# Kernel tuning notes

Hardware: AMD Instinct MI355X
Metric: run time of the kernel (lower is better)

## Reference

```python
import jax, jax.numpy as jnp
import numpy as np
import math

H = 128          # num heads
D = 5120         # hidden
Q_LORA = 1536
KV_LORA = 512    # nope_size / latent dim
ROPE = 64        # qk_rope_head_dim
NOPE = 128       # qk_nope_head_dim
VDIM = 128       # v_head_dim
Q_HEAD = NOPE + ROPE  # 192
EPS = 1e-6
_MSCALE = 0.1 * 1.0 * math.log(40.0) + 1.0
SCALE = (Q_HEAD ** -0.5) * _MSCALE * _MSCALE


def rmsnorm(x, w):
    var = jnp.mean(x.astype(jnp.float32) ** 2, axis=-1, keepdims=True)
    return (x * jax.lax.rsqrt(var + EPS)).astype(x.dtype) * w


def rotate_half(x):
    h = x.shape[-1] // 2
    return jnp.concatenate([-x[..., h:], x[..., :h]], axis=-1)


def apply_rope(x, cos, sin):
    return x * cos + rotate_half(x) * sin


def setup_inputs() -> dict:
    key = jax.random.key(0)
    ks = jax.random.split(key, 12)
    S = 1024
    s = 0.02
    return {
        'hidden_states': jax.random.normal(ks[0], (1, S, D), jnp.float32),
        'cos': jax.random.uniform(ks[1], (S, ROPE), jnp.float32, -1.0, 1.0),
        'sin': jax.random.uniform(ks[2], (S, ROPE), jnp.float32, -1.0, 1.0),
        'q_a_w': jax.random.normal(ks[3], (D, Q_LORA), jnp.float32) * s,
        'q_a_ln_w': jnp.ones((Q_LORA,), jnp.float32),
        'q_b_w': jax.random.normal(ks[4], (Q_LORA, H * Q_HEAD), jnp.float32) * s,
        'kv_a_w': jax.random.normal(ks[5], (D, KV_LORA + ROPE), jnp.float32) * s,
        'kv_a_ln_w': jnp.ones((KV_LORA,), jnp.float32),
        'kc_w': jax.random.normal(ks[6], (H, NOPE, KV_LORA), jnp.float32) * s,
        'vc_w': jax.random.normal(ks[7], (H, KV_LORA, VDIM), jnp.float32) * s,
        'o_w': jax.random.normal(ks[8], (H * VDIM, D), jnp.float32) * s,
    }


def reference(hidden_states, cos, sin, q_a_w, q_a_ln_w, q_b_w, kv_a_w,
              kv_a_ln_w, kc_w, vc_w, o_w):
    h = hidden_states[0]                     # [S, D]
    S = h.shape[0]

    # --- q path: low-rank q with RMSNorm, then absorbed nope proj via per-head bmm
    q = rmsnorm(h @ q_a_w, q_a_ln_w) @ q_b_w  # [S, H*192]
    q = q.reshape(S, H, Q_HEAD)
    q_nope, q_pe = q[..., :NOPE], q[..., NOPE:]         # [S,H,128], [S,H,64]
    q_nope_abs = jnp.einsum('shd,hdl->shl', q_nope, kc_w)  # [S,H,512] (kc bmm)

    # --- kv path: shared latent (MQA, 1 kv head)
    kv = h @ kv_a_w                          # [S, 512+64]
    k_pe = kv[:, KV_LORA:]                   # [S, 64]
    latent = rmsnorm(kv[:, :KV_LORA], kv_a_ln_w)  # [S, 512] = value states

    # --- partial RoPE on the 64-dim pe slice only
    q_pe = apply_rope(q_pe, cos[:, None, :], sin[:, None, :])
    k_pe = apply_rope(k_pe, cos, sin)

    q_full = jnp.concatenate([q_nope_abs, q_pe], axis=-1)  # [S,H,576]
    k_full = jnp.concatenate([latent, k_pe], axis=-1)      # [S,576]

    # --- causal MLA attention in latent space (values = 512-dim latent)
    scores = jnp.einsum('qhd,kd->hqk', q_full, k_full) * SCALE  # [H,S,S]
    causal = jnp.tril(jnp.ones((S, S), bool))
    scores = jnp.where(causal[None], scores, jnp.finfo(scores.dtype).min)
    probs = jax.nn.softmax(scores, axis=-1)
    attn = jnp.einsum('hqk,kl->qhl', probs, latent)         # [S,H,512]

    # --- vc bmm back to v_head_dim, then output proj
    out = jnp.einsum('shl,hlv->shv', attn, vc_w)            # [S,H,128]
    out = out.reshape(S, H * VDIM) @ o_w                    # [S, D]
    return out[None]                                        # [1,S,D]
```

## Files before the change

### kernel.cpp

```cpp
#include <hip/hip_runtime.h>
#include <hip/hip_bf16.h>
#include <math.h>

#define S_LEN  1024
#define DMODEL 5120
#define QLORA  1536
#define KVLORA 512
#define ROPE_D 64
#define NOPE_D 128
#define VDIM_D 128
#define QHEAD  192
#define NHEAD  128

typedef __hip_bfloat16 bf16;

using bf16x8 = __attribute__((ext_vector_type(8))) __bf16;
using f32x4  = __attribute__((ext_vector_type(4))) float;

__device__ __forceinline__ float toF(float x) { return x; }
__device__ __forceinline__ float toF(bf16 x)  { return __bfloat162float(x); }

__device__ __forceinline__ bf16x8 ld8(const bf16* p) {
  return *reinterpret_cast<const bf16x8*>(p);
}

__global__ __launch_bounds__(256) void cvt_bf16(const float* __restrict__ in,
                                                bf16* __restrict__ out) {
  const int i = (blockIdx.x * 256 + threadIdx.x) * 4;
  const float4 v = *reinterpret_cast<const float4*>(in + i);
  out[i + 0] = __float2bfloat16(v.x);
  out[i + 1] = __float2bfloat16(v.y);
  out[i + 2] = __float2bfloat16(v.z);
  out[i + 3] = __float2bfloat16(v.w);
}

__global__ __launch_bounds__(256) void transpose_w(const float* __restrict__ in,
                                                   bf16* __restrict__ out,
                                                   int R, int C) {
  __shared__ float tile[32][33];
  const int h = blockIdx.z;
  const int c0 = blockIdx.x * 32, r0 = blockIdx.y * 32;
  const int rr = threadIdx.x >> 3, cc = (threadIdx.x & 7) * 4;
  const float* ip = in + ((size_t)h * R + r0 + rr) * C + c0 + cc;
#pragma unroll
  for (int i = 0; i < 4; ++i) tile[rr][cc + i] = ip[i];
  __syncthreads();
  bf16* op = out + ((size_t)h * C + c0 + rr) * R + r0 + cc;
#pragma unroll
  for (int i = 0; i < 4; ++i) op[i] = __float2bfloat16(tile[cc + i][rr]);
}

template<int MODE>
__global__ __launch_bounds__(256) void gemm_mfma(const bf16* __restrict__ A,
                                                 const bf16* __restrict__ BT,
                                                 void* __restrict__ Cout,
                                                 int M, int N, int K) {
  __shared__ bf16 As[128][72];
  __shared__ bf16 Bs[128][72];
  const int n0 = blockIdx.x * 128, m0 = blockIdx.y * 128;
  const int tid = threadIdx.x;
  const int w = tid >> 6, l = tid & 63, lr = l & 15, lg = l >> 4;
  const int wr = w >> 1, wc = w & 1;

  f32x4 acc[4][4];
#pragma unroll
  for (int x = 0; x < 4; ++x)
#pragma unroll
    for (int y = 0; y < 4; ++y) acc[x][y] = (f32x4){0.f, 0.f, 0.f, 0.f};

  for (int kk = 0; kk < K; kk += 64) {
#pragma unroll
    for (int i = 0; i < 4; ++i) {
      const int e = tid + 256 * i;
      const int r = e >> 3, k8 = (e & 7) * 8;
      *reinterpret_cast<bf16x8*>(&As[r][k8]) =
          ld8(A + (size_t)(m0 + r) * K + kk + k8);
      const int bn = (n0 + r < N) ? n0 + r : N - 1;
      *reinterpret_cast<bf16x8*>(&Bs[r][k8]) =
          ld8(BT + (size_t)bn * K + kk + k8);
    }
    __syncthreads();
#pragma unroll
    for (int kh = 0; kh < 2; ++kh) {
      bf16x8 af[4], bg[4];
#pragma unroll
      for (int x = 0; x < 4; ++x) af[x] = ld8(&As[wr * 64 + x * 16 + lr][kh * 32 + lg * 8]);
#pragma unroll
      for (int y = 0; y < 4; ++y) bg[y] = ld8(&Bs[wc * 64 + y * 16 + lr][kh * 32 + lg * 8]);
#pragma unroll
      for (int x = 0; x < 4; ++x)
#pragma unroll
        for (int y = 0; y < 4; ++y)
          acc[x][y] = __builtin_amdgcn_mfma_f32_16x16x32_bf16(af[x], bg[y], acc[x][y], 0, 0, 0);
    }
    __syncthreads();
  }

#pragma unroll
  for (int x = 0; x < 4; ++x) {
    const int mb = m0 + wr * 64 + x * 16 + lg * 4;
#pragma unroll
    for (int y = 0; y < 4; ++y) {
      const int n = n0 + wc * 64 + y * 16 + lr;
      if (n < N) {
#pragma unroll
        for (int i = 0; i < 4; ++i) {
          const int m = mb + i;
          if (MODE == 0) {
            ((float*)Cout)[(size_t)m * N + n] = acc[x][y][i];
          } else if (MODE == 1) {
            ((bf16*)Cout)[(size_t)m * N + n] = __float2bfloat16(acc[x][y][i]);
          } else {
            const int h = n / QHEAD, j = n - h * QHEAD;
            ((bf16*)Cout)[((size_t)h * S_LEN + m) * QHEAD + j] = __float2bfloat16(acc[x][y][i]);
          }
        }
      }
    }
  }
}

__global__ __launch_bounds__(256) void rmsnorm_kernel(const bf16* __restrict__ in,
                                                      const float* __restrict__ w,
                                                      bf16* __restrict__ out, int N) {
  const int row = blockIdx.x, tid = threadIdx.x;
  __shared__ float red[256];
  float ss = 0.f;
  for (int c = tid; c < N; c += 256) { float x = toF(in[(size_t)row * N + c]); ss += x * x; }
  red[tid] = ss; __syncthreads();
  for (int s = 128; s > 0; s >>= 1) { if (tid < s) red[tid] += red[tid + s]; __syncthreads(); }
  const float rs = rsqrtf(red[0] / (float)N + 1e-6f);
  for (int c = tid; c < N; c += 256) {
    float x = toF(in[(size_t)row * N + c]);
    out[(size_t)row * N + c] = __float2bfloat16(x * rs * w[c]);
  }
}

__global__ __launch_bounds__(256) void kfull_kernel(const float* __restrict__ kv,
                                                    const float* __restrict__ w,
                                                    const float* __restrict__ cosb,
                                                    const float* __restrict__ sinb,
                                                    bf16* __restrict__ kfull) {
  const int s = blockIdx.x, tid = threadIdx.x;
  __shared__ float red[256];
  const float* row = kv + (size_t)s * 576;
  const float x0 = row[tid], x1 = row[256 + tid];
  red[tid] = x0 * x0 + x1 * x1; __syncthreads();
  for (int t = 128; t > 0; t >>= 1) { if (tid < t) red[tid] += red[tid + t]; __syncthreads(); }
  const float rs = rsqrtf(red[0] / 512.f + 1e-6f);
  bf16* krow = kfull + (size_t)s * 576;
  krow[tid]       = __float2bfloat16(x0 * rs * w[tid]);
  krow[256 + tid] = __float2bfloat16(x1 * rs * w[256 + tid]);
  if (tid < 32) {
    const int j = tid;
    const float a = row[512 + j], b = row[544 + j];
    const float* cs = cosb + (size_t)s * 64;
    const float* sn = sinb + (size_t)s * 64;
    krow[512 + j] = __float2bfloat16(a * cs[j] - b * sn[j]);
    krow[544 + j] = __float2bfloat16(b * cs[32 + j] + a * sn[32 + j]);
  }
}

__global__ __launch_bounds__(256) void rope_q_kernel(bf16* __restrict__ qperm,
                                                     const float* __restrict__ cosb,
                                                     const float* __restrict__ sinb) {
  const int idx = blockIdx.x * 256 + threadIdx.x;
  const int h = idx >> 15;
  const int rem = idx & 32767;
  const int s = rem >> 5;
  const int j = rem & 31;
  bf16* base = qperm + ((size_t)h * S_LEN + s) * QHEAD + NOPE_D;
  const float a = toF(base[j]), b = toF(base[32 + j]);
  const float* cs = cosb + (size_t)s * 64;
  const float* sn = sinb + (size_t)s * 64;
  base[j]      = __float2bfloat16(a * cs[j] - b * sn[j]);
  base[32 + j] = __float2bfloat16(b * cs[32 + j] + a * sn[32 + j]);
}

__global__ __launch_bounds__(256) void latT_kernel(const bf16* __restrict__ kfull,
                                                   bf16* __restrict__ latT) {
  const int gid = blockIdx.x * 256 + threadIdx.x;
  const int v = gid >> 10, s = gid & 1023;
  latT[gid] = kfull[(size_t)s * 576 + v];
}

#define QB 32
__global__ __launch_bounds__(256, 3) void attn_mfma(const bf16* __restrict__ qperm,
                                                    const bf16* __restrict__ kfull,
                                                    const bf16* __restrict__ kcT,
                                                    const bf16* __restrict__ vcT,
                                                    const bf16* __restrict__ latT,
                                                    bf16* __restrict__ attnv,
                                                    float scale) {
  const int bi = blockIdx.x;
  const int y  = bi >> 3;
  const int h  = (bi & 7) * 16 + (y >> 5);
  const int qb = y & 31;
  const int r0 = qb * QB;
  const int tid = threadIdx.x;
  const int w = tid >> 6, l = tid & 63, lr = l & 15, lg = l >> 4;

  __shared__ bf16  Qf[QB][584];
  __shared__ float St[QB][68];
  __shared__ bf16  Pt[QB][72];
  __shared__ float mrow[QB], lrow[QB], arow[QB];

  for (int e = tid; e < QB * 64; e += 256) {
    const int i = e >> 6, j = e & 63;
    Qf[i][512 + j] = qperm[((size_t)h * S_LEN + r0 + i) * QHEAD + NOPE_D + j];
  }
  {
    bf16x8 qn[2][4];
#pragma unroll
    for (int x = 0; x < 2; ++x) {
      const bf16* qp = qperm + ((size_t)h * S_LEN + r0 + x * 16 + lr) * QHEAD;
#pragma unroll
      for (int t = 0; t < 4; ++t) qn[x][t] = ld8(qp + t * 32 + lg * 8);
    }
#pragma unroll
    for (int ff = 0; ff < 2; ++ff) {
      bf16x8 kb[4][4];
#pragma unroll
      for (int f4 = 0; f4 < 4; ++f4) {
        const int col = w * 128 + (ff * 4 + f4) * 16 + lr;
        const bf16* kp = kcT + ((size_t)h * 512 + col) * 128 + lg * 8;
#pragma unroll
        for (int t = 0; t < 4; ++t) kb[f4][t] = ld8(kp + t * 32);
      }
#pragma unroll
      for (int f4 = 0; f4 < 4; ++f4) {
        f32x4 a0 = {0.f, 0.f, 0.f, 0.f}, a1 = {0.f, 0.f, 0.f, 0.f};
        const int col = w * 128 + (ff * 4 + f4) * 16 + lr;
#pragma unroll
        for (int t = 0; t < 4; ++t) {
          a0 = __builtin_amdgcn_mfma_f32_16x16x32_bf16(qn[0][t], kb[f4][t], a0, 0, 0, 0);
          a1 = __builtin_amdgcn_mfma_f32_16x16x32_bf16(qn[1][t], kb[f4][t], a1, 0, 0, 0);
        }
#pragma unroll
        for (int i = 0; i < 4; ++i) {
          Qf[lg * 4 + i][col]      = __float2bfloat16(a0[i]);
          Qf[16 + lg * 4 + i][col] = __float2bfloat16(a1[i]);
        }
      }
    }
  }
  if (tid < QB) { mrow[tid] = -INFINITY; lrow[tid] = 0.f; }
  __syncthreads();

  f32x4 o[2][8];
#pragma unroll
  for (int x = 0; x < 2; ++x)
#pragma unroll
    for (int f = 0; f < 8; ++f) o[x][f] = (f32x4){0.f, 0.f, 0.f, 0.f};

  const int kend = r0 + QB;
  for (int k0 = 0; k0 < kend; k0 += 64) {
    {
      const int key = k0 + w * 16 + lr;
      const bf16* kp = kfull + (size_t)key * 576 + lg * 8;
      bf16x8 bb[18];
#pragma unroll
      for (int t = 0; t < 18; ++t) bb[t] = ld8(kp + t * 32);
      f32x4 s0 = {0.f, 0.f, 0.f, 0.f}, s1 = {0.f, 0.f, 0.f, 0.f};
      __builtin_amdgcn_s_setprio(1);
#pragma unroll
      for (int t = 0; t < 18; ++t) {
        s0 = __builtin_amdgcn_mfma_f32_16x16x32_bf16(ld8(&Qf[lr][t * 32 + lg * 8]), bb[t], s0, 0, 0, 0);
        s1 = __builtin_amdgcn_mfma_f32_16x16x32_bf16(ld8(&Qf[16 + lr][t * 32 + lg * 8]), bb[t], s1, 0, 0, 0);
      }
      __builtin_amdgcn_s_setprio(0);
#pragma unroll
      for (int i = 0; i < 4; ++i) {
        const int q0 = r0 + lg * 4 + i;
        const int q1 = r0 + 16 + lg * 4 + i;
        St[lg * 4 + i][w * 16 + lr]      = (key <= q0) ? s0[i] * scale : -INFINITY;
        St[16 + lg * 4 + i][w * 16 + lr] = (key <= q1) ? s1[i] * scale : -INFINITY;
      }
    }
    __syncthreads();
    {
      const int r = tid >> 3, seg = tid & 7;
      const float4 v0 = *reinterpret_cast<const float4*>(&St[r][seg * 8]);
      const float4 v1 = *reinterpret_cast<const float4*>(&St[r][seg * 8 + 4]);
      float mx = fmaxf(fmaxf(fmaxf(v0.x, v0.y), fmaxf(v0.z, v0.w)),
                       fmaxf(fmaxf(v1.x, v1.y), fmaxf(v1.z, v1.w)));
#pragma unroll
      for (int m = 1; m < 8; m <<= 1) mx = fmaxf(mx, __shfl_xor(mx, m, 64));
      const float mold = mrow[r];
      const float mnew = fmaxf(mold, mx);
      const float p0 = expf(v0.x - mnew), p1 = expf(v0.y - mnew);
      const float p2 = expf(v0.z - mnew), p3 = expf(v0.w - mnew);
      const float p4 = expf(v1.x - mnew), p5 = expf(v1.y - mnew);
      const float p6 = expf(v1.z - mnew), p7 = expf(v1.w - mnew);
      Pt[r][seg * 8 + 0] = __float2bfloat16(p0);
      Pt[r][seg * 8 + 1] = __float2bfloat16(p1);
      Pt[r][seg * 8 + 2] = __float2bfloat16(p2);
      Pt[r][seg * 8 + 3] = __float2bfloat16(p3);
      Pt[r][seg * 8 + 4] = __float2bfloat16(p4);
      Pt[r][seg * 8 + 5] = __float2bfloat16(p5);
      Pt[r][seg * 8 + 6] = __float2bfloat16(p6);
      Pt[r][seg * 8 + 7] = __float2bfloat16(p7);
      float sum = p0 + p1 + p2 + p3 + p4 + p5 + p6 + p7;
#pragma unroll
      for (int m = 1; m < 8; m <<= 1) sum += __shfl_xor(sum, m, 64);
      if (seg == 0) {
        const float alpha = expf(mold - mnew);
        lrow[r] = lrow[r] * alpha + sum;
        mrow[r] = mnew;
        arow[r] = alpha;
      }
    }
    __syncthreads();
    {
      bf16x8 bl[16];
#pragma unroll
      for (int f = 0; f < 8; ++f) {
        const int v = w * 128 + f * 16 + lr;
        const bf16* bp = latT + (size_t)v * S_LEN + k0 + lg * 8;
        bl[2 * f]     = ld8(bp);
        bl[2 * f + 1] = ld8(bp + 32);
      }
      float al0[4], al1[4];
#pragma unroll
      for (int i = 0; i < 4; ++i) {
        al0[i] = arow[lg * 4 + i];
        al1[i] = arow[16 + lg * 4 + i];
      }
#pragma unroll
      for (int f = 0; f < 8; ++f)
#pragma unroll
        for (int i = 0; i < 4; ++i) {
          o[0][f][i] *= al0[i];
          o[1][f][i] *= al1[i];
        }
      bf16x8 pa[2][2];
      pa[0][0] = ld8(&Pt[lr][lg * 8]);
      pa[0][1] = ld8(&Pt[lr][32 + lg * 8]);
      pa[1][0] = ld8(&Pt[16 + lr][lg * 8]);
      pa[1][1] = ld8(&Pt[16 + lr][32 + lg * 8]);
      __builtin_amdgcn_s_setprio(1);
#pragma unroll
      for (int f = 0; f < 8; ++f) {
        o[0][f] = __builtin_amdgcn_mfma_f32_16x16x32_bf16(pa[0][0], bl[2 * f],     o[0][f], 0, 0, 0);
        o[0][f] = __builtin_amdgcn_mfma_f32_16x16x32_bf16(pa[0][1], bl[2 * f + 1], o[0][f], 0, 0, 0);
        o[1][f] = __builtin_amdgcn_mfma_f32_16x16x32_bf16(pa[1][0], bl[2 * f],     o[1][f], 0, 0, 0);
        o[1][f] = __builtin_amdgcn_mfma_f32_16x16x32_bf16(pa[1][1], bl[2 * f + 1], o[1][f], 0, 0, 0);
      }
      __builtin_amdgcn_s_setprio(0);
    }
  }

  {
    float li0[4], li1[4];
#pragma unroll
    for (int i = 0; i < 4; ++i) {
      li0[i] = 1.f / lrow[lg * 4 + i];
      li1[i] = 1.f / lrow[16 + lg * 4 + i];
    }
#pragma unroll
    for (int f = 0; f < 8; ++f) {
      const int v = w * 128 + f * 16 + lr;
#pragma unroll
      for (int i = 0; i < 4; ++i) {
        Qf[lg * 4 + i][v]      = __float2bfloat16(o[0][f][i] * li0[i]);
        Qf[16 + lg * 4 + i][v] = __float2bfloat16(o[1][f][i] * li1[i]);
      }
    }
  }
  __syncthreads();
#pragma unroll
  for (int cf = 0; cf < 2; ++cf) {
    const int c = w * 32 + cf * 16 + lr;
    const bf16* vp = vcT + ((size_t)h * 128 + c) * 512 + lg * 8;
    bf16x8 vb[16];
#pragma unroll
    for (int kt = 0; kt < 16; ++kt) vb[kt] = ld8(vp + kt * 32);
    f32x4 acc0 = {0.f, 0.f, 0.f, 0.f}, acc1 = {0.f, 0.f, 0.f, 0.f};
#pragma unroll
    for (int kt = 0; kt < 16; ++kt) {
      acc0 = __builtin_amdgcn_mfma_f32_16x16x32_bf16(ld8(&Qf[lr][kt * 32 + lg * 8]), vb[kt], acc0, 0, 0, 0);
      acc1 = __builtin_amdgcn_mfma_f32_16x16x32_bf16(ld8(&Qf[16 + lr][kt * 32 + lg * 8]), vb[kt], acc1, 0, 0, 0);
    }
#pragma unroll
    for (int i = 0; i < 4; ++i) {
      attnv[(size_t)(r0 + lg * 4 + i) * (NHEAD * VDIM_D) + h * VDIM_D + c]      = __float2bfloat16(acc0[i]);
      attnv[(size_t)(r0 + 16 + lg * 4 + i) * (NHEAD * VDIM_D) + h * VDIM_D + c] = __float2bfloat16(acc1[i]);
    }
  }
}

extern "C" void kernel_launch(void* const* d_in, const int* in_sizes, int n_in,
                              void* d_out, int out_size, void* d_ws, size_t ws_size,
                              hipStream_t stream) {
  const float* hidden    = (const float*)d_in[0];
  const float* cosb      = (const float*)d_in[1];
  const float* sinb      = (const float*)d_in[2];
  const float* q_a_w     = (const float*)d_in[3];
  const float* q_a_ln_w  = (const float*)d_in[4];
  const float* q_b_w     = (const float*)d_in[5];
  const float* kv_a_w    = (const float*)d_in[6];
  const float* kv_a_ln_w = (const float*)d_in[7];
  const float* kc_w      = (const float*)d_in[8];
  const float* vc_w      = (const float*)d_in[9];
  const float* o_w       = (const float*)d_in[10];
  float* out = (float*)d_out;

  char* ws = (char*)d_ws;
  bf16*  hb    = (bf16*)(ws + 0);
  bf16*  qaT   = (bf16*)(ws + 10485760);
  bf16*  kvaT  = (bf16*)(ws + 26214400);
  bf16*  kcT   = (bf16*)(ws + 32112640);
  bf16*  vcT   = (bf16*)(ws + 48889856);
  bf16*  kfull = (bf16*)(ws + 65667072);
  bf16*  latT  = (bf16*)(ws + 66846720);
  bf16*  qa    = (bf16*)(ws + 67895296);
  bf16*  qan   = (bf16*)(ws + 71041024);
  float* kv    = (float*)(ws + 74186752);
  bf16*  qperm = (bf16*)(ws + 76546048);
  bf16*  qbT   = (bf16*)(ws + 126877696);
  bf16*  attnv = (bf16*)(ws + 202375168);
  bf16*  owT   = (bf16*)(ws + 0);

  const double msc = 0.1 * log(40.0) + 1.0;
  const float scale = (float)(pow((double)QHEAD, -0.5) * msc * msc);

  cvt_bf16<<<(S_LEN * DMODEL) / 1024, 256, 0, stream>>>(hidden, hb);
  transpose_w<<<dim3(QLORA / 32, DMODEL / 32, 1), 256, 0, stream>>>(q_a_w, qaT, DMODEL, QLORA);
  transpose_w<<<dim3(576 / 32, DMODEL / 32, 1), 256, 0, stream>>>(kv_a_w, kvaT, DMODEL, 576);
  transpose_w<<<dim3((NHEAD * QHEAD) / 32, QLORA / 32, 1), 256, 0, stream>>>(q_b_w, qbT, QLORA, NHEAD * QHEAD);
  transpose_w<<<dim3(512 / 32, 128 / 32, NHEAD), 256, 0, stream>>>(kc_w, kcT, 128, 512);
  transpose_w<<<dim3(128 / 32, 512 / 32, NHEAD), 256, 0, stream>>>(vc_w, vcT, 512, 128);

  gemm_mfma<1><<<dim3(QLORA / 128, S_LEN / 128), 256, 0, stream>>>(
      hb, qaT, qa, S_LEN, QLORA, DMODEL);
  rmsnorm_kernel<<<S_LEN, 256, 0, stream>>>(qa, q_a_ln_w, qan, QLORA);
  gemm_mfma<2><<<dim3((NHEAD * QHEAD) / 128, S_LEN / 128), 256, 0, stream>>>(
      qan, qbT, qperm, S_LEN, NHEAD * QHEAD, QLORA);
  gemm_mfma<0><<<dim3(5, S_LEN / 128), 256, 0, stream>>>(
      hb, kvaT, kv, S_LEN, KVLORA + ROPE_D, DMODEL);
  kfull_kernel<<<S_LEN, 256, 0, stream>>>(kv, kv_a_ln_w, cosb, sinb, kfull);
  latT_kernel<<<(KVLORA * S_LEN) / 256, 256, 0, stream>>>(kfull, latT);
  rope_q_kernel<<<(NHEAD * S_LEN * 32) / 256, 256, 0, stream>>>(qperm, cosb, sinb);
  attn_mfma<<<dim3(NHEAD * (S_LEN / QB)), 256, 0, stream>>>(
      qperm, kfull, kcT, vcT, latT, attnv, scale);
  transpose_w<<<dim3(DMODEL / 32, (NHEAD * VDIM_D) / 32, 1), 256, 0, stream>>>(
      o_w, owT, NHEAD * VDIM_D, DMODEL);
  gemm_mfma<0><<<dim3(DMODEL / 128, S_LEN / 128), 256, 0, stream>>>(
      attnv, owT, out, S_LEN, DMODEL, NHEAD * VDIM_D);
}
```

Before: 2.192 ms.

## Split-K the q_a, kv_a and output GEMMs and fuse partial reductions

Adds a split-K mode to the MFMA GEMM that writes fp32 partial sums per K slice, and uses it for the q_a (8-way), kv_a (16-way) and output (2-way) projections. These launches otherwise have few tiles (96, 40 and 320 blocks) on a chip with many CUs. The partials are summed inside the RMSNorm and k_full kernels, plus a separate reduction kernel for the output. The workspace layout is reshuffled so partial buffers alias later-use regions. The cost is extra fp32 partial traffic and one extra reduction kernel for the output.

```diff
diff --git a/kernel.cpp b/kernel.cpp
--- a/kernel.cpp
+++ b/kernel.cpp
@@ -50,7 +50,7 @@
   for (int i = 0; i < 4; ++i) op[i] = __float2bfloat16(tile[cc + i][rr]);
 }
 
-template<int MODE>
+template<int MODE, int SPLIT = 1>
 __global__ __launch_bounds__(256) void gemm_mfma(const bf16* __restrict__ A,
                                                  const bf16* __restrict__ BT,
                                                  void* __restrict__ Cout,
@@ -58,6 +58,9 @@
   __shared__ bf16 As[128][72];
   __shared__ bf16 Bs[128][72];
   const int n0 = blockIdx.x * 128, m0 = blockIdx.y * 128;
+  const int z  = (SPLIT > 1) ? blockIdx.z : 0;
+  const int Ks = K / SPLIT;
+  const int kbeg = z * Ks;
   const int tid = threadIdx.x;
   const int w = tid >> 6, l = tid & 63, lr = l & 15, lg = l >> 4;
   const int wr = w >> 1, wc = w & 1;
@@ -68,7 +71,7 @@
 #pragma unroll
     for (int y = 0; y < 4; ++y) acc[x][y] = (f32x4){0.f, 0.f, 0.f, 0.f};
 
-  for (int kk = 0; kk < K; kk += 64) {
+  for (int kk = kbeg; kk < kbeg + Ks; kk += 64) {
 #pragma unroll
     for (int i = 0; i < 4; ++i) {
       const int e = tid + 256 * i;
@@ -110,9 +113,11 @@
             ((float*)Cout)[(size_t)m * N + n] = acc[x][y][i];
           } else if (MODE == 1) {
             ((bf16*)Cout)[(size_t)m * N + n] = __float2bfloat16(acc[x][y][i]);
-          } else {
+          } else if (MODE == 2) {
             const int h = n / QHEAD, j = n - h * QHEAD;
             ((bf16*)Cout)[((size_t)h * S_LEN + m) * QHEAD + j] = __float2bfloat16(acc[x][y][i]);
+          } else {
+            ((float*)Cout)[(size_t)z * M * N + (size_t)m * N + n] = acc[x][y][i];
           }
         }
       }
@@ -120,31 +125,44 @@
   }
 }
 
-__global__ __launch_bounds__(256) void rmsnorm_kernel(const bf16* __restrict__ in,
-                                                      const float* __restrict__ w,
-                                                      bf16* __restrict__ out, int N) {
+__global__ __launch_bounds__(256) void rmsnorm_fused(const float* __restrict__ part,
+                                                     const float* __restrict__ w,
+                                                     bf16* __restrict__ out) {
   const int row = blockIdx.x, tid = threadIdx.x;
   __shared__ float red[256];
+  float x[6];
   float ss = 0.f;
-  for (int c = tid; c < N; c += 256) { float x = toF(in[(size_t)row * N + c]); ss += x * x; }
+#pragma unroll
+  for (int j = 0; j < 6; ++j) {
+    const int c = tid + 256 * j;
+    float s = 0.f;
+#pragma unroll
+    for (int z = 0; z < 8; ++z) s += part[((size_t)z * S_LEN + row) * QLORA + c];
+    x[j] = s; ss += s * s;
+  }
   red[tid] = ss; __syncthreads();
-  for (int s = 128; s > 0; s >>= 1) { if (tid < s) red[tid] += red[tid + s]; __syncthreads(); }
-  const float rs = rsqrtf(red[0] / (float)N + 1e-6f);
-  for (int c = tid; c < N; c += 256) {
-    float x = toF(in[(size_t)row * N + c]);
-    out[(size_t)row * N + c] = __float2bfloat16(x * rs * w[c]);
-  }
-}
-
-__global__ __launch_bounds__(256) void kfull_kernel(const float* __restrict__ kv,
-                                                    const float* __restrict__ w,
-                                                    const float* __restrict__ cosb,
-                                                    const float* __restrict__ sinb,
-                                                    bf16* __restrict__ kfull) {
+  for (int t = 128; t > 0; t >>= 1) { if (tid < t) red[tid] += red[tid + t]; __syncthreads(); }
+  const float rs = rsqrtf(red[0] / (float)QLORA + 1e-6f);
+#pragma unroll
+  for (int j = 0; j < 6; ++j) {
+    const int c = tid + 256 * j;
+    out[(size_t)row * QLORA + c] = __float2bfloat16(x[j] * rs * w[c]);
+  }
+}
+
+__global__ __launch_bounds__(256) void kfull_fused(const float* __restrict__ part,
+                                                   const float* __restrict__ w,
+                                                   const float* __restrict__ cosb,
+                                                   const float* __restrict__ sinb,
+                                                   bf16* __restrict__ kfull) {
   const int s = blockIdx.x, tid = threadIdx.x;
   __shared__ float red[256];
-  const float* row = kv + (size_t)s * 576;
-  const float x0 = row[tid], x1 = row[256 + tid];
+  float x0 = 0.f, x1 = 0.f;
+#pragma unroll
+  for (int z = 0; z < 16; ++z) {
+    const float* row = part + ((size_t)z * S_LEN + s) * 576;
+    x0 += row[tid]; x1 += row[256 + tid];
+  }
   red[tid] = x0 * x0 + x1 * x1; __syncthreads();
   for (int t = 128; t > 0; t >>= 1) { if (tid < t) red[tid] += red[tid + t]; __syncthreads(); }
   const float rs = rsqrtf(red[0] / 512.f + 1e-6f);
@@ -153,12 +171,26 @@
   krow[256 + tid] = __float2bfloat16(x1 * rs * w[256 + tid]);
   if (tid < 32) {
     const int j = tid;
-    const float a = row[512 + j], b = row[544 + j];
+    float a = 0.f, b = 0.f;
+#pragma unroll
+    for (int z = 0; z < 16; ++z) {
+      const float* row = part + ((size_t)z * S_LEN + s) * 576;
+      a += row[512 + j]; b += row[544 + j];
+    }
     const float* cs = cosb + (size_t)s * 64;
     const float* sn = sinb + (size_t)s * 64;
     krow[512 + j] = __float2bfloat16(a * cs[j] - b * sn[j]);
     krow[544 + j] = __float2bfloat16(b * cs[32 + j] + a * sn[32 + j]);
   }
+}
+
+__global__ __launch_bounds__(256) void reduce2_f32(const float* __restrict__ p,
+                                                   float* __restrict__ out) {
+  const size_t i = ((size_t)blockIdx.x * 256 + threadIdx.x) * 4;
+  const float4 a = *reinterpret_cast<const float4*>(p + i);
+  const float4 b = *reinterpret_cast<const float4*>(p + (size_t)S_LEN * DMODEL + i);
+  float4 r; r.x = a.x + b.x; r.y = a.y + b.y; r.z = a.z + b.z; r.w = a.w + b.w;
+  *reinterpret_cast<float4*>(out + i) = r;
 }
 
 __global__ __launch_bounds__(256) void rope_q_kernel(bf16* __restrict__ qperm,
@@ -406,20 +438,21 @@
   float* out = (float*)d_out;
 
   char* ws = (char*)d_ws;
-  bf16*  hb    = (bf16*)(ws + 0);
-  bf16*  qaT   = (bf16*)(ws + 10485760);
-  bf16*  kvaT  = (bf16*)(ws + 26214400);
-  bf16*  kcT   = (bf16*)(ws + 32112640);
-  bf16*  vcT   = (bf16*)(ws + 48889856);
-  bf16*  kfull = (bf16*)(ws + 65667072);
-  bf16*  latT  = (bf16*)(ws + 66846720);
-  bf16*  qa    = (bf16*)(ws + 67895296);
-  bf16*  qan   = (bf16*)(ws + 71041024);
-  float* kv    = (float*)(ws + 74186752);
-  bf16*  qperm = (bf16*)(ws + 76546048);
-  bf16*  qbT   = (bf16*)(ws + 126877696);
-  bf16*  attnv = (bf16*)(ws + 202375168);
-  bf16*  owT   = (bf16*)(ws + 0);
+  bf16*  attnv   = (bf16*)(ws + 0);
+  bf16*  kcT     = (bf16*)(ws + 33554432);
+  bf16*  vcT     = (bf16*)(ws + 50331648);
+  bf16*  kfull   = (bf16*)(ws + 67108864);
+  bf16*  latT    = (bf16*)(ws + 68288512);
+  bf16*  qan     = (bf16*)(ws + 69337088);
+  bf16*  hb      = (bf16*)(ws + 72482816);
+  bf16*  qaT     = (bf16*)(ws + 82968576);
+  bf16*  kvaT    = (bf16*)(ws + 98697216);
+  bf16*  qperm   = (bf16*)(ws + 104595456);
+  float* qa_part = (float*)(ws + 104595456);
+  bf16*  qbT     = (bf16*)(ws + 154927104);
+  float* kv_part = (float*)(ws + 154927104);
+  float* o_part  = (float*)(ws + 33554432);
+  bf16*  owT     = (bf16*)(ws + 75497472);
 
   const double msc = 0.1 * log(40.0) + 1.0;
   const float scale = (float)(pow((double)QHEAD, -0.5) * msc * msc);
@@ -431,20 +464,21 @@
   transpose_w<<<dim3(512 / 32, 128 / 32, NHEAD), 256, 0, stream>>>(kc_w, kcT, 128, 512);
   transpose_w<<<dim3(128 / 32, 512 / 32, NHEAD), 256, 0, stream>>>(vc_w, vcT, 512, 128);
 
-  gemm_mfma<1><<<dim3(QLORA / 128, S_LEN / 128), 256, 0, stream>>>(
-      hb, qaT, qa, S_LEN, QLORA, DMODEL);
-  rmsnorm_kernel<<<S_LEN, 256, 0, stream>>>(qa, q_a_ln_w, qan, QLORA);
+  gemm_mfma<3, 8><<<dim3(QLORA / 128, S_LEN / 128, 8), 256, 0, stream>>>(
+      hb, qaT, qa_part, S_LEN, QLORA, DMODEL);
+  rmsnorm_fused<<<S_LEN, 256, 0, stream>>>(qa_part, q_a_ln_w, qan);
   gemm_mfma<2><<<dim3((NHEAD * QHEAD) / 128, S_LEN / 128), 256, 0, stream>>>(
       qan, qbT, qperm, S_LEN, NHEAD * QHEAD, QLORA);
-  gemm_mfma<0><<<dim3(5, S_LEN / 128), 256, 0, stream>>>(
-      hb, kvaT, kv, S_LEN, KVLORA + ROPE_D, DMODEL);
-  kfull_kernel<<<S_LEN, 256, 0, stream>>>(kv, kv_a_ln_w, cosb, sinb, kfull);
+  gemm_mfma<3, 16><<<dim3(5, S_LEN / 128, 16), 256, 0, stream>>>(
+      hb, kvaT, kv_part, S_LEN, KVLORA + ROPE_D, DMODEL);
+  kfull_fused<<<S_LEN, 256, 0, stream>>>(kv_part, kv_a_ln_w, cosb, sinb, kfull);
   latT_kernel<<<(KVLORA * S_LEN) / 256, 256, 0, stream>>>(kfull, latT);
   rope_q_kernel<<<(NHEAD * S_LEN * 32) / 256, 256, 0, stream>>>(qperm, cosb, sinb);
   attn_mfma<<<dim3(NHEAD * (S_LEN / QB)), 256, 0, stream>>>(
       qperm, kfull, kcT, vcT, latT, attnv, scale);
   transpose_w<<<dim3(DMODEL / 32, (NHEAD * VDIM_D) / 32, 1), 256, 0, stream>>>(
       o_w, owT, NHEAD * VDIM_D, DMODEL);
-  gemm_mfma<0><<<dim3(DMODEL / 128, S_LEN / 128), 256, 0, stream>>>(
-      attnv, owT, out, S_LEN, DMODEL, NHEAD * VDIM_D);
-}
+  gemm_mfma<3, 2><<<dim3(DMODEL / 128, S_LEN / 128, 2), 256, 0, stream>>>(
+      attnv, owT, o_part, S_LEN, DMODEL, NHEAD * VDIM_D);
+  reduce2_f32<<<(S_LEN * DMODEL) / 1024, 256, 0, stream>>>(o_part, out);
+}
```

Measured after the change: 2.039 ms. 1.08x faster.
